# Performance work log

Measured on AMD Instinct MI355X. Metric: run time of the kernel, lower is better.

Reference implementation:

```python
import jax, jax.numpy as jnp
import numpy as np

N = 50000
NEG_SLOPE = 0.2
EPS = 1e-16


def add_self_loops(edge_index, n):
    loop = jnp.arange(n, dtype=edge_index.dtype)
    src = jnp.concatenate([edge_index[0], loop])
    dst = jnp.concatenate([edge_index[1], loop])
    return src, dst


def gat_conv(x, src, dst, W, att_src, att_dst, bias, n):
    # x: [N, F_in]; W: [F_in, H*D]; att_*: [H, D]; bias: [H*D]
    H, D = att_src.shape
    h = (x @ W).reshape(n, H, D)                      # [N, H, D]
    a_src = jnp.einsum('nhd,hd->nh', h, att_src)      # [N, H]
    a_dst = jnp.einsum('nhd,hd->nh', h, att_dst)
    e = jax.nn.leaky_relu(a_src[src] + a_dst[dst], NEG_SLOPE)  # [E, H]
    # softmax over incoming edges per destination node, per head
    m = jax.ops.segment_max(e, dst, num_segments=n)   # [N, H]
    ex = jnp.exp(e - m[dst])
    s = jax.ops.segment_sum(ex, dst, num_segments=n)
    alpha = ex / (s[dst] + EPS)                       # [E, H]
    msg = h[src] * alpha[:, :, None]                  # [E, H, D]
    out = jax.ops.segment_sum(msg, dst, num_segments=n)
    return out.reshape(n, H * D) + bias


def gcn_conv(x, src, dst, W, bias, n):
    h = x @ W                                         # [N, C]
    deg = jax.ops.segment_sum(jnp.ones_like(src, dtype=h.dtype), dst, num_segments=n)
    dinv = jnp.where(deg > 0, jax.lax.rsqrt(deg), 0.0)
    norm = dinv[src] * dinv[dst]                      # [E]
    out = jax.ops.segment_sum(h[src] * norm[:, None], dst, num_segments=n)
    return out + bias


def setup_inputs() -> dict:
    key = jax.random.key(0)
    ks = jax.random.split(key, 12)
    F_in, hid, heads, ncls = 128, 32, 8, 8
    d2 = hid // 2  # 16
    E = 500000
    x = jax.random.normal(ks[0], (N, F_in), dtype=jnp.float32)
    edge_index = jax.random.randint(ks[1], (2, E), 0, N, dtype=jnp.int32)
    sc = lambda k, sh: jax.random.normal(k, sh, dtype=jnp.float32) * 0.05
    return {
        'x': x, 'edge_index': edge_index,
        'W1': sc(ks[2], (F_in, heads * hid)),
        'att_src1': sc(ks[3], (heads, hid)), 'att_dst1': sc(ks[4], (heads, hid)),
        'b1': jnp.zeros((heads * hid,), jnp.float32),
        'W2': sc(ks[5], (heads * hid, heads * d2)),
        'att_src2': sc(ks[6], (heads, d2)), 'att_dst2': sc(ks[7], (heads, d2)),
        'b2': jnp.zeros((heads * d2,), jnp.float32),
        'Wg': sc(ks[8], (heads * d2, ncls)),
        'bg': jnp.zeros((ncls,), jnp.float32),
    }


def reference(x, edge_index, W1, att_src1, att_dst1, b1, W2, att_src2, att_dst2, b2, Wg, bg):
    src, dst = add_self_loops(edge_index, N)
    h = gat_conv(x, src, dst, W1, att_src1, att_dst1, b1, N)
    h = jax.nn.relu(h)
    h = gat_conv(h, src, dst, W2, att_src2, att_dst2, b2, N)
    h = jax.nn.relu(h)
    return gcn_conv(h, src, dst, Wg, bg, N)
```

## Files before the change

### kernel.cpp

```cpp
#include <hip/hip_runtime.h>
#include <hip/hip_bf16.h>


typedef __attribute__((ext_vector_type(8))) short bf16x8;
typedef __attribute__((ext_vector_type(4))) float f32x4;


__device__ __forceinline__ float4 bf4_to_f4(uint2 v) {
    float4 r;
    r.x = __uint_as_float((v.x & 0xFFFFu) << 16);
    r.y = __uint_as_float(v.x & 0xFFFF0000u);
    r.z = __uint_as_float((v.y & 0xFFFFu) << 16);
    r.w = __uint_as_float(v.y & 0xFFFF0000u);
    return r;
}

__device__ __forceinline__ ushort f_to_bf(float f) {
    __hip_bfloat16 hb = __float2bfloat16(f);
    return *reinterpret_cast<ushort*>(&hb);
}


__global__ __launch_bounds__(256) void prep_kernel(
    const float* __restrict__ x,
    const float* __restrict__ W1, const float* __restrict__ as1, const float* __restrict__ ad1,
    const float* __restrict__ W2, const float* __restrict__ as2, const float* __restrict__ ad2,
    ushort* __restrict__ xb, ushort* __restrict__ W1t, ushort* __restrict__ W2t,
    float* __restrict__ w1s, float* __restrict__ w1d,
    float* __restrict__ w2s, float* __restrict__ w2d,
    int* __restrict__ deg, int n) {
    const int tid = blockIdx.x * 256 + threadIdx.x;
    const int NT = gridDim.x * 256;
    for (int i = tid; i < n; i += NT) deg[i] = 0;
    for (int j = tid; j < n * 32; j += NT) {
        int i = j * 4;
        float4 v = *reinterpret_cast<const float4*>(x + i);
        ushort4 u = make_ushort4(f_to_bf(v.x), f_to_bf(v.y), f_to_bf(v.z), f_to_bf(v.w));
        *reinterpret_cast<ushort4*>(xb + i) = u;
    }
    for (int j = tid; j < 32768; j += NT) {
        int nn = j >> 7, k = j & 127;
        W1t[j] = f_to_bf(W1[(size_t)k * 256 + nn]);
    }
    for (int j = tid; j < 32768; j += NT) {
        int nn = j >> 8, k = j & 255;
        W2t[j] = f_to_bf(W2[(size_t)k * 128 + nn]);
    }
    for (int j = tid; j < 1024; j += NT) {
        int k = j >> 3, h = j & 7;
        const float* wrow = W1 + (size_t)k * 256 + h * 32;
        const float* as = as1 + h * 32;
        const float* ad = ad1 + h * 32;
        float s1 = 0.f, s2 = 0.f;
        #pragma unroll
        for (int d = 0; d < 32; d += 4) {
            float4 wv = *reinterpret_cast<const float4*>(wrow + d);
            float4 av = *reinterpret_cast<const float4*>(as + d);
            float4 dv = *reinterpret_cast<const float4*>(ad + d);
            s1 += wv.x * av.x + wv.y * av.y + wv.z * av.z + wv.w * av.w;
            s2 += wv.x * dv.x + wv.y * dv.y + wv.z * dv.z + wv.w * dv.w;
        }
        w1s[j] = s1; w1d[j] = s2;
    }
    for (int j = tid; j < 2048; j += NT) {
        int k = j >> 3, h = j & 7;
        const float* wrow = W2 + (size_t)k * 128 + h * 16;
        const float* as = as2 + h * 16;
        const float* ad = ad2 + h * 16;
        float s1 = 0.f, s2 = 0.f;
        #pragma unroll
        for (int d = 0; d < 16; d += 4) {
            float4 wv = *reinterpret_cast<const float4*>(wrow + d);
            float4 av = *reinterpret_cast<const float4*>(as + d);
            float4 dv = *reinterpret_cast<const float4*>(ad + d);
            s1 += wv.x * av.x + wv.y * av.y + wv.z * av.z + wv.w * av.w;
            s2 += wv.x * dv.x + wv.y * dv.y + wv.z * dv.z + wv.w * dv.w;
        }
        w2s[j] = s1; w2d[j] = s2;
    }
}


__global__ __launch_bounds__(256) void hist_adots_kernel(
    const int* __restrict__ ei, int E, int Etot, int* __restrict__ deg,
    const ushort* __restrict__ xb,
    const float* __restrict__ w1s, const float* __restrict__ w1d,
    float* __restrict__ a_s, float* __restrict__ a_d, int n) {
    const int tid = blockIdx.x * 256 + threadIdx.x;
    const int NT = gridDim.x * 256;
    for (int e = tid; e < Etot; e += NT) {
        int d = (e < E) ? ei[E + e] : (e - E);
        atomicAdd(&deg[d], 1);
    }
    for (int j = tid; j < n * 8; j += NT) {
        int node = j >> 3, h = j & 7;
        const ushort* xp = xb + (size_t)node * 128;
        float s1 = 0.f, s2 = 0.f;
        #pragma unroll 4
        for (int k = 0; k < 128; k += 8) {
            uint4 v = *reinterpret_cast<const uint4*>(xp + k);
            float4 x0 = bf4_to_f4(make_uint2(v.x, v.y));
            float4 x1 = bf4_to_f4(make_uint2(v.z, v.w));
            s1 += x0.x * w1s[(k + 0) * 8 + h] + x0.y * w1s[(k + 1) * 8 + h] +
                  x0.z * w1s[(k + 2) * 8 + h] + x0.w * w1s[(k + 3) * 8 + h] +
                  x1.x * w1s[(k + 4) * 8 + h] + x1.y * w1s[(k + 5) * 8 + h] +
                  x1.z * w1s[(k + 6) * 8 + h] + x1.w * w1s[(k + 7) * 8 + h];
            s2 += x0.x * w1d[(k + 0) * 8 + h] + x0.y * w1d[(k + 1) * 8 + h] +
                  x0.z * w1d[(k + 2) * 8 + h] + x0.w * w1d[(k + 3) * 8 + h] +
                  x1.x * w1d[(k + 4) * 8 + h] + x1.y * w1d[(k + 5) * 8 + h] +
                  x1.z * w1d[(k + 6) * 8 + h] + x1.w * w1d[(k + 7) * 8 + h];
        }
        a_s[j] = s1;
        a_d[j] = s2;
    }
}


__global__ __launch_bounds__(256) void scanA_kernel(const int* __restrict__ deg,
                                                    int* __restrict__ off,
                                                    int* __restrict__ bsum, int n) {
    __shared__ int buf[256];
    int t = threadIdx.x;
    int i = blockIdx.x * 256 + t;
    int v = (i < n) ? deg[i] : 0;
    buf[t] = v;
    __syncthreads();
    #pragma unroll
    for (int st = 1; st < 256; st <<= 1) {
        int x = (t >= st) ? buf[t - st] : 0;
        __syncthreads();
        buf[t] += x;
        __syncthreads();
    }
    if (i < n) off[i + 1] = buf[t];
    if (t == 255) bsum[blockIdx.x] = buf[255];
}


__global__ __launch_bounds__(256) void scanC_kernel(const int* __restrict__ deg,
                                                    int* __restrict__ off,
                                                    const int* __restrict__ bsum,
                                                    int* __restrict__ cur,
                                                    float* __restrict__ dinv, int n) {
    __shared__ int sred[256];
    const int bid = blockIdx.x;
    const int t = threadIdx.x;
    sred[t] = (t < bid) ? bsum[t] : 0;
    __syncthreads();
    #pragma unroll
    for (int st = 128; st > 0; st >>= 1) {
        if (t < st) sred[t] += sred[t + st];
        __syncthreads();
    }
    const int pre = sred[0];
    int i = bid * 256 + t;
    if (i < n) {
        int o = off[i + 1] + pre;
        off[i + 1] = o;
        int d = deg[i];
        cur[i] = o - d;
        dinv[i] = rsqrtf((float)d);
    }
    if (i == 0) off[0] = 0;
}


__global__ __launch_bounds__(256) void scatter_kernel(const int* __restrict__ ei, int E, int Etot,
                                                      int* __restrict__ cur,
                                                      int* __restrict__ ssrc) {
    int e = blockIdx.x * 256 + threadIdx.x;
    if (e >= Etot) return;
    int s, d;
    if (e < E) { s = ei[e]; d = ei[E + e]; }
    else       { s = e - E; d = e - E; }
    int pos = atomicAdd(&cur[d], 1);
    ssrc[pos] = s;
}


template <int K>
__global__ __launch_bounds__(256) void adots_kernel(const ushort* __restrict__ Xb,
                                                    const float* __restrict__ ws,
                                                    const float* __restrict__ wd,
                                                    float* __restrict__ a_s,
                                                    float* __restrict__ a_d, int n) {
    int gid = blockIdx.x * 256 + threadIdx.x;
    if (gid >= n * 8) return;
    int node = gid >> 3, h = gid & 7;
    const ushort* xp = Xb + (size_t)node * K;
    float s1 = 0.f, s2 = 0.f;
    #pragma unroll 4
    for (int k = 0; k < K; k += 8) {
        uint4 v = *reinterpret_cast<const uint4*>(xp + k);
        float4 x0 = bf4_to_f4(make_uint2(v.x, v.y));
        float4 x1 = bf4_to_f4(make_uint2(v.z, v.w));
        s1 += x0.x * ws[(k + 0) * 8 + h] + x0.y * ws[(k + 1) * 8 + h] +
              x0.z * ws[(k + 2) * 8 + h] + x0.w * ws[(k + 3) * 8 + h] +
              x1.x * ws[(k + 4) * 8 + h] + x1.y * ws[(k + 5) * 8 + h] +
              x1.z * ws[(k + 6) * 8 + h] + x1.w * ws[(k + 7) * 8 + h];
        s2 += x0.x * wd[(k + 0) * 8 + h] + x0.y * wd[(k + 1) * 8 + h] +
              x0.z * wd[(k + 2) * 8 + h] + x0.w * wd[(k + 3) * 8 + h] +
              x1.x * wd[(k + 4) * 8 + h] + x1.y * wd[(k + 5) * 8 + h] +
              x1.z * wd[(k + 6) * 8 + h] + x1.w * wd[(k + 7) * 8 + h];
    }
    a_s[gid] = s1;
    a_d[gid] = s2;
}


template <int K, int NC, int BN>
__global__ __launch_bounds__(256) void mfma_gemm_kernel(const ushort* __restrict__ Ab,
                                                        const ushort* __restrict__ Bt,
                                                        ushort* __restrict__ Cb, int M) {
    constexpr int BM = 128, BK = 32;
    constexpr int FN = BN / 32;
    __shared__ ushort As[BM * BK];
    __shared__ ushort Bs[BN * BK];
    const int tid = threadIdx.x;
    const int lane = tid & 63;
    const int wid = tid >> 6;
    const int bm = blockIdx.y * BM;
    const int bn = blockIdx.x * BN;
    const int wm = (wid >> 1) * 64;
    const int wn = (wid & 1) * (BN / 2);
    const int l15 = lane & 15;
    const int l4 = lane >> 4;
    f32x4 zero4 = {0.f, 0.f, 0.f, 0.f};
    f32x4 acc[4][FN];
    #pragma unroll
    for (int i = 0; i < 4; ++i)
        #pragma unroll
        for (int j = 0; j < FN; ++j) acc[i][j] = zero4;

    for (int k0 = 0; k0 < K; k0 += BK) {
        #pragma unroll
        for (int p = 0; p < 2; ++p) {
            int ci = tid + p * 256;
            int r = ci >> 2, c = ci & 3;
            int row = bm + r;
            uint4 v = make_uint4(0, 0, 0, 0);
            if (row < M) v = *reinterpret_cast<const uint4*>(&Ab[(size_t)row * K + k0 + c * 8]);
            *reinterpret_cast<uint4*>(&As[r * BK + c * 8]) = v;
        }
        #pragma unroll
        for (int p = 0; p < BN / 64; ++p) {
            int ci = tid + p * 256;
            int r = ci >> 2, c = ci & 3;
            uint4 v = *reinterpret_cast<const uint4*>(&Bt[(size_t)(bn + r) * K + k0 + c * 8]);
            *reinterpret_cast<uint4*>(&Bs[r * BK + c * 8]) = v;
        }
        __syncthreads();
        bf16x8 af[4], bfr[FN];
        #pragma unroll
        for (int i = 0; i < 4; ++i)
            af[i] = *reinterpret_cast<const bf16x8*>(&As[(wm + 16 * i + l15) * BK + l4 * 8]);
        #pragma unroll
        for (int j = 0; j < FN; ++j)
            bfr[j] = *reinterpret_cast<const bf16x8*>(&Bs[(wn + 16 * j + l15) * BK + l4 * 8]);
        #pragma unroll
        for (int i = 0; i < 4; ++i)
            #pragma unroll
            for (int j = 0; j < FN; ++j)
                acc[i][j] = __builtin_amdgcn_mfma_f32_16x16x32_bf16(af[i], bfr[j], acc[i][j], 0, 0, 0);
        __syncthreads();
    }
    #pragma unroll
    for (int i = 0; i < 4; ++i) {
        #pragma unroll
        for (int p = 0; p < 4; ++p) {
            int row = bm + wm + 16 * i + l4 * 4 + p;
            if (row < M) {
                #pragma unroll
                for (int j = 0; j < FN; ++j) {
                    Cb[(size_t)row * NC + bn + wn + 16 * j + l15] = f_to_bf(acc[i][j][p]);
                }
            }
        }
    }
}


#define LRELU_EXP(e) __expf((e) > 0.f ? (e) : 0.2f * (e))

template <int C, int DH>
__global__ __launch_bounds__(256) void gat_agg_kernel(const ushort* __restrict__ hfeat,
                                                      const float* __restrict__ a_src,
                                                      const float* __restrict__ a_dst,
                                                      const int* __restrict__ off,
                                                      const int* __restrict__ ssrc,
                                                      const float* __restrict__ bias,
                                                      ushort* __restrict__ outb, int n) {
    constexpr int LPN = C / 4;
    constexpr int GS = DH / 4;
    const int node = blockIdx.x * (256 / LPN) + threadIdx.x / LPN;
    if (node >= n) return;
    const int local = threadIdx.x & (LPN - 1);
    const int c0 = local * 4;
    const int h = c0 / DH;
    const int subl = local & (GS - 1);
    const float adst = a_dst[node * 8 + h];
    const int o0 = off[node], o1 = off[node + 1];
    float ax = 0.f, ay = 0.f, az = 0.f, aw = 0.f, ssum = 0.f;
    int i = o0;
    const int nfull = o0 + ((o1 - o0) / GS) * GS;
    for (; i < nfull; i += GS) {
        int smy = ssrc[i + subl];
        float e = a_src[smy * 8 + h] + adst;
        float evmy = LRELU_EXP(e);
        int sj[GS];
        #pragma unroll
        for (int j = 0; j < GS; ++j) sj[j] = __shfl(smy, j, GS);
        uint2 rv[GS];
        #pragma unroll
        for (int j = 0; j < GS; ++j)
            rv[j] = *reinterpret_cast<const uint2*>(&hfeat[(size_t)sj[j] * C + c0]);
        #pragma unroll
        for (int j = 0; j < GS; ++j) {
            float ev = __shfl(evmy, j, GS);
            float4 hv = bf4_to_f4(rv[j]);
            ssum += ev;
            ax += ev * hv.x; ay += ev * hv.y; az += ev * hv.z; aw += ev * hv.w;
        }
    }
    for (; i < o1; ++i) {
        int s = ssrc[i];
        float e = a_src[s * 8 + h] + adst;
        float v = LRELU_EXP(e);
        uint2 rvv = *reinterpret_cast<const uint2*>(&hfeat[(size_t)s * C + c0]);
        float4 hv = bf4_to_f4(rvv);
        ssum += v;
        ax += v * hv.x; ay += v * hv.y; az += v * hv.z; aw += v * hv.w;
    }
    float sinv = 1.f / (ssum + 1e-16f);
    float4 bb = *reinterpret_cast<const float4*>(bias + c0);
    float ox = fmaxf(ax * sinv + bb.x, 0.f);
    float oy = fmaxf(ay * sinv + bb.y, 0.f);
    float oz = fmaxf(az * sinv + bb.z, 0.f);
    float ow = fmaxf(aw * sinv + bb.w, 0.f);
    ushort4 u = make_ushort4(f_to_bf(ox), f_to_bf(oy), f_to_bf(oz), f_to_bf(ow));
    *reinterpret_cast<ushort4*>(&outb[(size_t)node * C + c0]) = u;
}


__global__ __launch_bounds__(256) void gcn_gemm_kernel(const ushort* __restrict__ Ab,
                                                       const float* __restrict__ Wg,
                                                       const float* __restrict__ dinv,
                                                       float* __restrict__ g, int n) {
    __shared__ float W[128 * 8];
    for (int i = threadIdx.x; i < 1024; i += 256) W[i] = Wg[i];
    __syncthreads();
    int gid = blockIdx.x * 256 + threadIdx.x;
    if (gid >= n * 8) return;
    int node = gid >> 3, c = gid & 7;
    const ushort* ap = Ab + (size_t)node * 128;
    float acc = 0.f;
    #pragma unroll
    for (int k = 0; k < 128; k += 8) {
        uint4 v = *reinterpret_cast<const uint4*>(ap + k);
        float4 x0 = bf4_to_f4(make_uint2(v.x, v.y));
        float4 x1 = bf4_to_f4(make_uint2(v.z, v.w));
        acc += x0.x * W[(k + 0) * 8 + c] + x0.y * W[(k + 1) * 8 + c] +
               x0.z * W[(k + 2) * 8 + c] + x0.w * W[(k + 3) * 8 + c] +
               x1.x * W[(k + 4) * 8 + c] + x1.y * W[(k + 5) * 8 + c] +
               x1.z * W[(k + 6) * 8 + c] + x1.w * W[(k + 7) * 8 + c];
    }
    g[gid] = acc * dinv[node];
}

__global__ __launch_bounds__(256) void gcn_agg_kernel(const float* __restrict__ g,
                                                      const float* __restrict__ dinv,
                                                      const int* __restrict__ off,
                                                      const int* __restrict__ ssrc,
                                                      const float* __restrict__ bg,
                                                      float* __restrict__ outp, int n) {
    int gid = blockIdx.x * 256 + threadIdx.x;
    if (gid >= n * 8) return;
    int node = gid >> 3, c = gid & 7;
    int o0 = off[node], o1 = off[node + 1];
    float acc = 0.f;
    for (int i = o0; i < o1; ++i) {
        int s = ssrc[i];
        acc += g[(size_t)s * 8 + c];
    }
    outp[gid] = acc * dinv[node] + bg[c];
}


extern "C" void kernel_launch(void* const* d_in, const int* in_sizes, int n_in,
                              void* d_out, int out_size, void* d_ws, size_t ws_size,
                              hipStream_t stream) {
    const float* x      = (const float*)d_in[0];
    const int*   ei     = (const int*)d_in[1];
    const float* W1     = (const float*)d_in[2];
    const float* att_s1 = (const float*)d_in[3];
    const float* att_d1 = (const float*)d_in[4];
    const float* b1     = (const float*)d_in[5];
    const float* W2     = (const float*)d_in[6];
    const float* att_s2 = (const float*)d_in[7];
    const float* att_d2 = (const float*)d_in[8];
    const float* b2     = (const float*)d_in[9];
    const float* Wg     = (const float*)d_in[10];
    const float* bg     = (const float*)d_in[11];
    float* out = (float*)d_out;

    const int n    = in_sizes[0] / 128;
    const int E    = in_sizes[1] / 2;
    const int Etot = E + n;

    float*  wsp   = (float*)d_ws;
    float*  regA  = wsp;
    float*  regB  = regA + (size_t)n * 128;
    float*  regC  = regB + (size_t)n * 128;
    float*  a_s   = regC + (size_t)n * 64;
    float*  a_d   = a_s + (size_t)n * 8;
    float*  g     = a_d + (size_t)n * 8;
    float*  dinv  = g + (size_t)n * 8;
    float*  w1s   = dinv + n;
    float*  w1d   = w1s + 1024;
    float*  w2s   = w1d + 1024;
    float*  w2d   = w2s + 2048;
    float*  w1t_f = w2d + 2048;
    float*  w2t_f = w1t_f + 16384;
    int*    off   = (int*)(w2t_f + 16384);
    int*    deg   = off + (n + 1);
    int*    cur   = deg + n;
    int*    ssrc  = cur + n;
    int*    bsum  = ssrc + Etot;

    ushort* h1b   = (ushort*)regA;
    ushort* out2b = (ushort*)regA;
    ushort* out1b = (ushort*)regB;
    ushort* xb    = (ushort*)regC;
    ushort* h2b   = (ushort*)regC;
    ushort* W1t   = (ushort*)w1t_f;
    ushort* W2t   = (ushort*)w2t_f;

    const dim3 b256(256);
    const int nch = (n + 255) / 256;

    prep_kernel<<<2048, b256, 0, stream>>>(x, W1, att_s1, att_d1, W2, att_s2, att_d2,
                                           xb, W1t, W2t, w1s, w1d, w2s, w2d, deg, n);
    hist_adots_kernel<<<2048, b256, 0, stream>>>(ei, E, Etot, deg, xb, w1s, w1d, a_s, a_d, n);
    scanA_kernel<<<nch, b256, 0, stream>>>(deg, off, bsum, n);
    scanC_kernel<<<nch, b256, 0, stream>>>(deg, off, bsum, cur, dinv, n);
    scatter_kernel<<<(Etot + 255) / 256, b256, 0, stream>>>(ei, E, Etot, cur, ssrc);

    mfma_gemm_kernel<128, 256, 128><<<dim3(2, (n + 127) / 128), b256, 0, stream>>>(xb, W1t, h1b, n);
    gat_agg_kernel<256, 32><<<(n + 3) / 4, b256, 0, stream>>>(h1b, a_s, a_d, off, ssrc, b1, out1b, n);

    adots_kernel<256><<<(n * 8 + 255) / 256, b256, 0, stream>>>(out1b, w2s, w2d, a_s, a_d, n);
    mfma_gemm_kernel<256, 128, 64><<<dim3(2, (n + 127) / 128), b256, 0, stream>>>(out1b, W2t, h2b, n);
    gat_agg_kernel<128, 16><<<(n + 7) / 8, b256, 0, stream>>>(h2b, a_s, a_d, off, ssrc, b2, out2b, n);

    gcn_gemm_kernel<<<(n * 8 + 255) / 256, b256, 0, stream>>>(out2b, Wg, dinv, g, n);
    gcn_agg_kernel<<<(n * 8 + 255) / 256, b256, 0, stream>>>(g, dinv, off, ssrc, bg, out, n);
}
```

Baseline: 241.1 us.

## Fuse independent kernels via block-range dispatch and fold GCN GEMM into GAT aggregation

The edge scatter now shares one launch with the first MFMA GEMM, and the layer-2 attention-dot kernel shares one launch with the second GEMM. Each fused kernel picks its role from the block index, so independent work runs concurrently and two launches are removed. The second GAT aggregation now applies the 128x8 GCN weight in-register, reduces across lanes with shuffles, and writes g directly, which removes the out2b round trip and the separate gcn_gemm launch. In exchange, the fused launches take the larger shared-memory footprint of the GEMM for every block, and the aggregation kernel does extra shuffle reductions.

After: 244.8 us. Within noise of the previous version (+1.5%).

```diff
diff --git a/kernel.cpp b/kernel.cpp
--- a/kernel.cpp
+++ b/kernel.cpp
@@ -19,6 +19,8 @@
     __hip_bfloat16 hb = __float2bfloat16(f);
     return *reinterpret_cast<ushort*>(&hb);
 }
+
+#define LRELU_EXP(e) __expf((e) > 0.f ? (e) : 0.2f * (e))
 
 
 __global__ __launch_bounds__(256) void prep_kernel(
@@ -165,62 +167,19 @@
 }
 
 
-__global__ __launch_bounds__(256) void scatter_kernel(const int* __restrict__ ei, int E, int Etot,
-                                                      int* __restrict__ cur,
-                                                      int* __restrict__ ssrc) {
-    int e = blockIdx.x * 256 + threadIdx.x;
-    if (e >= Etot) return;
-    int s, d;
-    if (e < E) { s = ei[e]; d = ei[E + e]; }
-    else       { s = e - E; d = e - E; }
-    int pos = atomicAdd(&cur[d], 1);
-    ssrc[pos] = s;
-}
-
-
-template <int K>
-__global__ __launch_bounds__(256) void adots_kernel(const ushort* __restrict__ Xb,
-                                                    const float* __restrict__ ws,
-                                                    const float* __restrict__ wd,
-                                                    float* __restrict__ a_s,
-                                                    float* __restrict__ a_d, int n) {
-    int gid = blockIdx.x * 256 + threadIdx.x;
-    if (gid >= n * 8) return;
-    int node = gid >> 3, h = gid & 7;
-    const ushort* xp = Xb + (size_t)node * K;
-    float s1 = 0.f, s2 = 0.f;
-    #pragma unroll 4
-    for (int k = 0; k < K; k += 8) {
-        uint4 v = *reinterpret_cast<const uint4*>(xp + k);
-        float4 x0 = bf4_to_f4(make_uint2(v.x, v.y));
-        float4 x1 = bf4_to_f4(make_uint2(v.z, v.w));
-        s1 += x0.x * ws[(k + 0) * 8 + h] + x0.y * ws[(k + 1) * 8 + h] +
-              x0.z * ws[(k + 2) * 8 + h] + x0.w * ws[(k + 3) * 8 + h] +
-              x1.x * ws[(k + 4) * 8 + h] + x1.y * ws[(k + 5) * 8 + h] +
-              x1.z * ws[(k + 6) * 8 + h] + x1.w * ws[(k + 7) * 8 + h];
-        s2 += x0.x * wd[(k + 0) * 8 + h] + x0.y * wd[(k + 1) * 8 + h] +
-              x0.z * wd[(k + 2) * 8 + h] + x0.w * wd[(k + 3) * 8 + h] +
-              x1.x * wd[(k + 4) * 8 + h] + x1.y * wd[(k + 5) * 8 + h] +
-              x1.z * wd[(k + 6) * 8 + h] + x1.w * wd[(k + 7) * 8 + h];
-    }
-    a_s[gid] = s1;
-    a_d[gid] = s2;
-}
-
-
 template <int K, int NC, int BN>
-__global__ __launch_bounds__(256) void mfma_gemm_kernel(const ushort* __restrict__ Ab,
-                                                        const ushort* __restrict__ Bt,
-                                                        ushort* __restrict__ Cb, int M) {
+__device__ __forceinline__ void gemm_body(const ushort* __restrict__ Ab,
+                                          const ushort* __restrict__ Bt,
+                                          ushort* __restrict__ Cb, int M,
+                                          int bxm, int bxn,
+                                          ushort* As, ushort* Bs) {
     constexpr int BM = 128, BK = 32;
     constexpr int FN = BN / 32;
-    __shared__ ushort As[BM * BK];
-    __shared__ ushort Bs[BN * BK];
     const int tid = threadIdx.x;
     const int lane = tid & 63;
     const int wid = tid >> 6;
-    const int bm = blockIdx.y * BM;
-    const int bn = blockIdx.x * BN;
+    const int bm = bxm * BM;
+    const int bn = bxn * BN;
     const int wm = (wid >> 1) * 64;
     const int wn = (wid & 1) * (BN / 2);
     const int l15 = lane & 15;
@@ -280,7 +239,61 @@
 }
 
 
-#define LRELU_EXP(e) __expf((e) > 0.f ? (e) : 0.2f * (e))
+__global__ __launch_bounds__(256) void scatter_gemm1_kernel(
+    const int* __restrict__ ei, int E, int Etot,
+    int* __restrict__ cur, int* __restrict__ ssrc,
+    const ushort* __restrict__ xb, const ushort* __restrict__ W1t,
+    ushort* __restrict__ h1b, int M, int ng) {
+    __shared__ ushort As[128 * 32];
+    __shared__ ushort Bs[128 * 32];
+    if ((int)blockIdx.x < ng) {
+        gemm_body<128, 256, 128>(xb, W1t, h1b, M, blockIdx.x >> 1, blockIdx.x & 1, As, Bs);
+    } else {
+        int e = (blockIdx.x - ng) * 256 + threadIdx.x;
+        if (e >= Etot) return;
+        int s, d;
+        if (e < E) { s = ei[e]; d = ei[E + e]; }
+        else       { s = e - E; d = e - E; }
+        int pos = atomicAdd(&cur[d], 1);
+        ssrc[pos] = s;
+    }
+}
+
+
+__global__ __launch_bounds__(256) void adots2_gemm2_kernel(
+    const ushort* __restrict__ out1b, const ushort* __restrict__ W2t,
+    ushort* __restrict__ h2b,
+    const float* __restrict__ w2s, const float* __restrict__ w2d,
+    float* __restrict__ a_s, float* __restrict__ a_d, int n, int ng) {
+    __shared__ ushort As[128 * 32];
+    __shared__ ushort Bs[64 * 32];
+    if ((int)blockIdx.x < ng) {
+        gemm_body<256, 128, 64>(out1b, W2t, h2b, n, blockIdx.x >> 1, blockIdx.x & 1, As, Bs);
+    } else {
+        int gid = (blockIdx.x - ng) * 256 + threadIdx.x;
+        if (gid >= n * 8) return;
+        int node = gid >> 3, h = gid & 7;
+        const ushort* xp = out1b + (size_t)node * 256;
+        float s1 = 0.f, s2 = 0.f;
+        #pragma unroll 4
+        for (int k = 0; k < 256; k += 8) {
+            uint4 v = *reinterpret_cast<const uint4*>(xp + k);
+            float4 x0 = bf4_to_f4(make_uint2(v.x, v.y));
+            float4 x1 = bf4_to_f4(make_uint2(v.z, v.w));
+            s1 += x0.x * w2s[(k + 0) * 8 + h] + x0.y * w2s[(k + 1) * 8 + h] +
+                  x0.z * w2s[(k + 2) * 8 + h] + x0.w * w2s[(k + 3) * 8 + h] +
+                  x1.x * w2s[(k + 4) * 8 + h] + x1.y * w2s[(k + 5) * 8 + h] +
+                  x1.z * w2s[(k + 6) * 8 + h] + x1.w * w2s[(k + 7) * 8 + h];
+            s2 += x0.x * w2d[(k + 0) * 8 + h] + x0.y * w2d[(k + 1) * 8 + h] +
+                  x0.z * w2d[(k + 2) * 8 + h] + x0.w * w2d[(k + 3) * 8 + h] +
+                  x1.x * w2d[(k + 4) * 8 + h] + x1.y * w2d[(k + 5) * 8 + h] +
+                  x1.z * w2d[(k + 6) * 8 + h] + x1.w * w2d[(k + 7) * 8 + h];
+        }
+        a_s[gid] = s1;
+        a_d[gid] = s2;
+    }
+}
+
 
 template <int C, int DH>
 __global__ __launch_bounds__(256) void gat_agg_kernel(const ushort* __restrict__ hfeat,
@@ -342,30 +355,80 @@
 }
 
 
-__global__ __launch_bounds__(256) void gcn_gemm_kernel(const ushort* __restrict__ Ab,
-                                                       const float* __restrict__ Wg,
-                                                       const float* __restrict__ dinv,
-                                                       float* __restrict__ g, int n) {
-    __shared__ float W[128 * 8];
-    for (int i = threadIdx.x; i < 1024; i += 256) W[i] = Wg[i];
+__global__ __launch_bounds__(256) void gat_agg2_gcn_kernel(
+    const ushort* __restrict__ hfeat,
+    const float* __restrict__ a_src, const float* __restrict__ a_dst,
+    const int* __restrict__ off, const int* __restrict__ ssrc,
+    const float* __restrict__ bias, const float* __restrict__ Wg,
+    const float* __restrict__ dinv, float* __restrict__ g, int n) {
+    constexpr int C = 128, DH = 16;
+    constexpr int LPN = C / 4;
+    constexpr int GS = DH / 4;
+    __shared__ float Wsh[128 * 8];
+    for (int i = threadIdx.x; i < 1024; i += 256) Wsh[i] = Wg[i];
     __syncthreads();
-    int gid = blockIdx.x * 256 + threadIdx.x;
-    if (gid >= n * 8) return;
-    int node = gid >> 3, c = gid & 7;
-    const ushort* ap = Ab + (size_t)node * 128;
-    float acc = 0.f;
+    const int node = blockIdx.x * (256 / LPN) + threadIdx.x / LPN;
+    if (node >= n) return;
+    const int local = threadIdx.x & (LPN - 1);
+    const int c0 = local * 4;
+    const int h = c0 / DH;
+    const int subl = local & (GS - 1);
+    const float adst = a_dst[node * 8 + h];
+    const int o0 = off[node], o1 = off[node + 1];
+    float ax = 0.f, ay = 0.f, az = 0.f, aw = 0.f, ssum = 0.f;
+    int i = o0;
+    const int nfull = o0 + ((o1 - o0) / GS) * GS;
+    for (; i < nfull; i += GS) {
+        int smy = ssrc[i + subl];
+        float e = a_src[smy * 8 + h] + adst;
+        float evmy = LRELU_EXP(e);
+        int sj[GS];
+        #pragma unroll
+        for (int j = 0; j < GS; ++j) sj[j] = __shfl(smy, j, GS);
+        uint2 rv[GS];
+        #pragma unroll
+        for (int j = 0; j < GS; ++j)
+            rv[j] = *reinterpret_cast<const uint2*>(&hfeat[(size_t)sj[j] * C + c0]);
+        #pragma unroll
+        for (int j = 0; j < GS; ++j) {
+            float ev = __shfl(evmy, j, GS);
+            float4 hv = bf4_to_f4(rv[j]);
+            ssum += ev;
+            ax += ev * hv.x; ay += ev * hv.y; az += ev * hv.z; aw += ev * hv.w;
+        }
+    }
+    for (; i < o1; ++i) {
+        int s = ssrc[i];
+        float e = a_src[s * 8 + h] + adst;
+        float v = LRELU_EXP(e);
+        uint2 rvv = *reinterpret_cast<const uint2*>(&hfeat[(size_t)s * C + c0]);
+        float4 hv = bf4_to_f4(rvv);
+        ssum += v;
+        ax += v * hv.x; ay += v * hv.y; az += v * hv.z; aw += v * hv.w;
+    }
+    float sinv = 1.f / (ssum + 1e-16f);
+    float4 bb = *reinterpret_cast<const float4*>(bias + c0);
+    float ox = fmaxf(ax * sinv + bb.x, 0.f);
+    float oy = fmaxf(ay * sinv + bb.y, 0.f);
+    float oz = fmaxf(az * sinv + bb.z, 0.f);
+    float ow = fmaxf(aw * sinv + bb.w, 0.f);
+    float p[8];
     #pragma unroll
-    for (int k = 0; k < 128; k += 8) {
-        uint4 v = *reinterpret_cast<const uint4*>(ap + k);
-        float4 x0 = bf4_to_f4(make_uint2(v.x, v.y));
-        float4 x1 = bf4_to_f4(make_uint2(v.z, v.w));
-        acc += x0.x * W[(k + 0) * 8 + c] + x0.y * W[(k + 1) * 8 + c] +
-               x0.z * W[(k + 2) * 8 + c] + x0.w * W[(k + 3) * 8 + c] +
-               x1.x * W[(k + 4) * 8 + c] + x1.y * W[(k + 5) * 8 + c] +
-               x1.z * W[(k + 6) * 8 + c] + x1.w * W[(k + 7) * 8 + c];
-    }
-    g[gid] = acc * dinv[node];
-}
+    for (int j = 0; j < 8; ++j)
+        p[j] = ox * Wsh[(c0 + 0) * 8 + j] + oy * Wsh[(c0 + 1) * 8 + j] +
+               oz * Wsh[(c0 + 2) * 8 + j] + ow * Wsh[(c0 + 3) * 8 + j];
+    #pragma unroll
+    for (int m = 1; m < LPN; m <<= 1) {
+        #pragma unroll
+        for (int j = 0; j < 8; ++j) p[j] += __shfl_xor(p[j], m);
+    }
+    if (local == 0) {
+        float dv = dinv[node];
+        *reinterpret_cast<float4*>(&g[node * 8]) = make_float4(p[0] * dv, p[1] * dv, p[2] * dv, p[3] * dv);
+        *reinterpret_cast<float4*>(&g[node * 8 + 4]) = make_float4(p[4] * dv, p[5] * dv, p[6] * dv, p[7] * dv);
+    }
+}
+
 
 __global__ __launch_bounds__(256) void gcn_agg_kernel(const float* __restrict__ g,
                                                       const float* __restrict__ dinv,
@@ -428,7 +491,6 @@
     int*    bsum  = ssrc + Etot;
 
     ushort* h1b   = (ushort*)regA;
-    ushort* out2b = (ushort*)regA;
     ushort* out1b = (ushort*)regB;
     ushort* xb    = (ushort*)regC;
     ushort* h2b   = (ushort*)regC;
@@ -443,15 +505,18 @@
     hist_adots_kernel<<<2048, b256, 0, stream>>>(ei, E, Etot, deg, xb, w1s, w1d, a_s, a_d, n);
     scanA_kernel<<<nch, b256, 0, stream>>>(deg, off, bsum, n);
     scanC_kernel<<<nch, b256, 0, stream>>>(deg, off, bsum, cur, dinv, n);
-    scatter_kernel<<<(Etot + 255) / 256, b256, 0, stream>>>(ei, E, Etot, cur, ssrc);
-
-    mfma_gemm_kernel<128, 256, 128><<<dim3(2, (n + 127) / 128), b256, 0, stream>>>(xb, W1t, h1b, n);
+
+    const int ng1 = 2 * ((n + 127) / 128);
+    scatter_gemm1_kernel<<<ng1 + (Etot + 255) / 256, b256, 0, stream>>>(
+        ei, E, Etot, cur, ssrc, xb, W1t, h1b, n, ng1);
+
     gat_agg_kernel<256, 32><<<(n + 3) / 4, b256, 0, stream>>>(h1b, a_s, a_d, off, ssrc, b1, out1b, n);
 
-    adots_kernel<256><<<(n * 8 + 255) / 256, b256, 0, stream>>>(out1b, w2s, w2d, a_s, a_d, n);
-    mfma_gemm_kernel<256, 128, 64><<<dim3(2, (n + 127) / 128), b256, 0, stream>>>(out1b, W2t, h2b, n);
-    gat_agg_kernel<128, 16><<<(n + 7) / 8, b256, 0, stream>>>(h2b, a_s, a_d, off, ssrc, b2, out2b, n);
-
-    gcn_gemm_kernel<<<(n * 8 + 255) / 256, b256, 0, stream>>>(out2b, Wg, dinv, g, n);
+    const int ng2 = 2 * ((n + 127) / 128);
+    adots2_gemm2_kernel<<<ng2 + (n * 8 + 255) / 256, b256, 0, stream>>>(
+        out1b, W2t, h2b, w2s, w2d, a_s, a_d, n, ng2);
+
+    gat_agg2_gcn_kernel<<<(n + 7) / 8, b256, 0, stream>>>(h2b, a_s, a_d, off, ssrc, b2, Wg, dinv, g, n);
+
     gcn_agg_kernel<<<(n * 8 + 255) / 256, b256, 0, stream>>>(g, dinv, off, ssrc, bg, out, n);
 }
```
